# Kernel tuning notes

Measured on AMD Instinct MI355X. Metric: run time of the kernel, lower is better.

Reference implementation:

```python
import jax, jax.numpy as jnp
from jax import lax
import numpy as np

B, T = 32, 15
THR1, THR2 = 15.0, 10.0  # conv1_t, conv2_t


def _conv(x, w):
    # x: (B,T,C,H,W) cumulative potentials/spikes; conv applied per timestep
    b, t, c, h, wd = x.shape
    y = lax.conv_general_dilated(x.reshape(b * t, c, h, wd), w, (1, 1), 'VALID',
                                 dimension_numbers=('NCHW', 'OIHW', 'NCHW'))
    return y.reshape(b, t, *y.shape[1:])


def _pool(x, k, s):
    b, t, c, h, wd = x.shape
    y = lax.reduce_window(x.reshape(b * t, c, h, wd), -jnp.inf, lax.max,
                          (1, 1, k, k), (1, 1, s, s), 'VALID')
    return y.reshape(b, t, *y.shape[1:])


def _pad(x, p):
    return jnp.pad(x, ((0, 0), (0, 0), (0, 0), (p, p), (p, p)))


def _fire(pot, thr):
    # sf.fire: F.threshold_(pot, thr, 0); spk = sign
    th = jnp.where(pot > thr, pot, 0.0)
    return jnp.sign(th), th


def _winner_class(pot, spk):
    # sf.get_k_winners(pot, kwta=1, r=0, spk): earliest spike, tie-break by potential
    b, t = spk.shape[:2]
    cnt = spk.sum(axis=1)                                   # (B,F,H,W) spike counts
    first = jnp.clip((t - cnt).astype(jnp.int32), 0, t - 1)  # earliest spike time
    vals = jnp.take_along_axis(pot, first[:, None], axis=1)[:, 0]  # pot at spike time
    trunc = spk * vals[:, None]                              # (B,T,F,H,W)
    v = trunc.reshape(b, -1).max(axis=1) * t                 # dominance offset per sample
    total = (trunc + spk * v[:, None, None, None, None]).sum(axis=1)  # (B,F,H,W)
    flat = total.reshape(b, -1)
    idx = jnp.argmax(flat, axis=1)
    mx = jnp.max(flat, axis=1)
    hw = pot.shape[-1] * pot.shape[-2]
    feat = idx // hw
    # decision_map: 10 classes x 20 features each -> class = feat // 20; -1 if no spike
    return jnp.where(mx != 0, feat // 20, -1).astype(jnp.int32)


def setup_inputs() -> dict:
    key = jax.random.key(0)
    k1, k2, k3, k4 = jax.random.split(key, 4)
    # cumulative binary spike wave: neuron fires at t_fire and stays 1 afterwards
    t_fire = jax.random.randint(k1, (B, 18, 32, 32), 0, T + 1)
    inp = (jnp.arange(T)[None, :, None, None, None] >= t_fire[:, None]).astype(jnp.float32)
    w1 = 0.8 + 0.05 * jax.random.normal(k2, (90, 18, 7, 7), dtype=jnp.float32)
    w2 = 0.8 + 0.05 * jax.random.normal(k3, (250, 90, 5, 5), dtype=jnp.float32)
    w3 = 0.8 + 0.05 * jax.random.normal(k4, (200, 250, 5, 5), dtype=jnp.float32)
    return {'input': inp, 'w1': w1, 'w2': w2, 'w3': w3, 'max_layer': 3}


def reference(input, w1, w2, w3, max_layer):
    # eval-mode forward of CIFAR10Net
    x = _pad(input, 2)                       # (B,T,18,36,36)
    spk1, pot1 = _fire(_conv(x, w1), THR1)   # (B,T,90,30,30)
    if max_layer == 1:
        return spk1, pot1
    spk2, pot2 = _fire(_conv(_pad(_pool(spk1, 2, 2), 1), w2), THR2)  # (B,T,250,13,13)
    if max_layer == 2:
        return spk2, pot2
    pot3 = _conv(_pad(_pool(spk2, 3, 3), 2), w3)   # (B,T,200,4,4)
    t = pot3.shape[1]
    mask = (jnp.arange(t) == t - 1).astype(pot3.dtype)[None, :, None, None, None]
    spk3 = jnp.sign(pot3 * mask)             # fire with threshold=None: only last step
    cls = _winner_class(pot3, spk3)          # (B,) predicted class or -1
    return cls, pot3
```

## Files before the change

kernel.cpp:

```cpp
#include <hip/hip_runtime.h>

#define NB 32
#define NT 15


__device__ __forceinline__ float gather8(const int* lst, int i, const char* wb) {
    int4 p0 = *(const int4*)(lst + i);
    int4 p1 = *(const int4*)(lst + i + 4);
    int o0 = __builtin_amdgcn_readfirstlane(p0.x);
    int o1 = __builtin_amdgcn_readfirstlane(p0.y);
    int o2 = __builtin_amdgcn_readfirstlane(p0.z);
    int o3 = __builtin_amdgcn_readfirstlane(p0.w);
    int o4 = __builtin_amdgcn_readfirstlane(p1.x);
    int o5 = __builtin_amdgcn_readfirstlane(p1.y);
    int o6 = __builtin_amdgcn_readfirstlane(p1.z);
    int o7 = __builtin_amdgcn_readfirstlane(p1.w);
    float a0 = *(const float*)(wb + o0);
    float a1 = *(const float*)(wb + o1);
    float a2 = *(const float*)(wb + o2);
    float a3 = *(const float*)(wb + o3);
    float a4 = *(const float*)(wb + o4);
    float a5 = *(const float*)(wb + o5);
    float a6 = *(const float*)(wb + o6);
    float a7 = *(const float*)(wb + o7);
    return ((a0 + a1) + (a2 + a3)) + ((a4 + a5) + (a6 + a7));
}

__device__ __forceinline__ void tr_tile(const float* __restrict__ src, float* __restrict__ dst,
                                        int F, int K, int KK, int CIN, int nkt, int t, int tid) {
    __shared__ float lds[32][33];
    int kt = t % nkt, ft = t / nkt;
    int k0 = kt * 32, f0 = ft * 32;
    int tx = tid & 31, ty = tid >> 5;
#pragma unroll
    for (int i = 0; i < 4; i++) {
        int fl = ty + 8 * i;
        int f = f0 + fl, k = k0 + tx;
        lds[fl][tx] = (f < F && k < K) ? src[(size_t)f * K + k] : 0.f;
    }
    __syncthreads();
#pragma unroll
    for (int i = 0; i < 4; i++) {
        int row = ty + 8 * i;
        int k = k0 + row, f = f0 + tx;
        if (k < K && f < F) {
            int j = (k % KK) * CIN + k / KK;
            dst[(size_t)j * F + f] = lds[tx][row];
        }
    }
}

__global__ __launch_bounds__(256) void k_pre(const float* __restrict__ inp,
                                             const float* __restrict__ w1,
                                             const float* __restrict__ w2,
                                             const float* __restrict__ w3,
                                             float* __restrict__ wT1, float* __restrict__ wT2,
                                             float* __restrict__ wT3,
                                             unsigned char* __restrict__ zmap,
                                             float* __restrict__ PosS2, float* __restrict__ PosS3,
                                             float* __restrict__ Pmin1,
                                             unsigned char* __restrict__ ft1,
                                             unsigned char* __restrict__ nzc1) {
    int blk = blockIdx.x, tid = threadIdx.x;
    if (blk < 2024) {
        const float* src; float* dst;
        int F, K, KK, CIN, nkt, t;
        if (blk < 84)       { src = w1; dst = wT1; F = 90;  K = 882;  KK = 49; CIN = 18;  nkt = 28;  t = blk; }
        else if (blk < 652) { src = w2; dst = wT2; F = 250; K = 2250; KK = 25; CIN = 90;  nkt = 71;  t = blk - 84; }
        else                { src = w3; dst = wT3; F = 200; K = 6250; KK = 25; CIN = 250; nkt = 196; t = blk - 652; }
        tr_tile(src, dst, F, K, KK, CIN, nkt, t, tid);
    } else if (blk == 2024) {
        if (tid < 90)  wT1[882 * 90 + tid] = 0.f;
        if (tid < 250) wT2[(size_t)2250 * 250 + tid] = 0.f;
        if (tid < 200) wT3[(size_t)6250 * 200 + tid] = 0.f;
    } else if (blk < 2187) {
        int idx = (blk - 2025) * 256 + tid;
        int xx = idx % 36, rest = idx / 36;
        int yy = rest % 36; int b = rest / 36;
        int z = 0;
        int x = xx - 2, y = yy - 2;
        if (x >= 0 && x < 32 && y >= 0 && y < 32) {
            const float* p = inp + (size_t)b * NT * 18 * 1024 + y * 32 + x;
#pragma unroll
            for (int c = 0; c < 18; c++) z += (p[(size_t)c * 1024] != 0.f);
        }
        zmap[idx] = (unsigned char)z;
    } else if (blk < 2212) {
        int idx = (blk - 2187) * 256 + tid;
        if (idx < 6250) {
            int f = idx / 25, pos = idx - f * 25;
            float acc = 0.f;
            for (int c = 0; c < 90; c++) acc += w2[(size_t)(f * 90 + c) * 25 + pos];
            PosS2[pos * 256 + f] = acc;
        }
    } else if (blk < 2232) {
        int idx = (blk - 2212) * 256 + tid;
        if (idx < 5000) {
            int f = idx / 25, pos = idx - f * 25;
            float acc = 0.f;
            for (int c = 0; c < 250; c++) acc += w3[(size_t)(f * 250 + c) * 25 + pos];
            PosS3[pos * 200 + f] = acc;
        }
    } else if (blk < 2272) {
        int bb = blk - 2232;
        __shared__ float wm[4];
        float m = 1e30f;
#pragma unroll
        for (int k = 0; k < 8; k++) {
            int i = bb * 2048 + k * 256 + tid;
            if (i < 90 * 882) m = fminf(m, w1[i]);
        }
        for (int o = 32; o > 0; o >>= 1) m = fminf(m, __shfl_down(m, o));
        if ((tid & 63) == 0) wm[tid >> 6] = m;
        __syncthreads();
        if (tid == 0) Pmin1[bb] = fminf(fminf(wm[0], wm[1]), fminf(wm[2], wm[3]));
    } else if (blk < 2905) {
        int i = (blk - 2272) * 256 + tid;
        if (i < 162000) ((uint4*)ft1)[i] = uint4{0, 0, 0, 0};
    } else {
        int i = (blk - 2905) * 256 + tid;
        if (i < 1800) ((uint4*)nzc1)[i] = uint4{0, 0, 0, 0};
    }
}

__global__ __launch_bounds__(256) void k_conv1(const float* __restrict__ inp,
                                               const unsigned char* __restrict__ zmap,
                                               const float* __restrict__ Pmin1,
                                               const float* __restrict__ wT1,
                                               const float* __restrict__ PosS2,
                                               const float* __restrict__ PosS3,
                                               unsigned char* __restrict__ ft1,
                                               unsigned char* __restrict__ nzc1,
                                               float* __restrict__ W2e,
                                               unsigned char* __restrict__ ft2,
                                               unsigned char* __restrict__ nzc2,
                                               float* __restrict__ W3s) {
    __shared__ __align__(16) int slist[896];
    __shared__ int scnt, spcnt, cnt0s;
    __shared__ float sm1;
    int blk = blockIdx.x, tid = threadIdx.x;
    if (blk < 28800) {
        int b = blk / 900, p = blk - b * 900;
        int oy = p / 30, ox = p - oy * 30;
        int zv = 0;
        if (tid < 49) zv = zmap[(b * 36 + oy + tid / 7) * 36 + ox + tid % 7];
        float mm = (tid < 40) ? Pmin1[tid] : 1e30f;
        if (tid < 64) {
            for (int o = 32; o > 0; o >>= 1) {
                zv += __shfl_down(zv, o);
                mm = fminf(mm, __shfl_down(mm, o));
            }
            if (tid == 0) { cnt0s = zv; sm1 = mm; }
        }
        __syncthreads();
        if ((float)cnt0s * sm1 > 15.0f) return;
        unsigned char myft[4];
#pragma unroll
        for (int k = 0; k < 4; k++) {
            int j = tid + k * 256;
            unsigned char v = 255;
            if (j < 882) {
                int dy = j / 126, rem = j - dy * 126;
                int dx = rem / 18, c = rem - dx * 18;
                int y = oy + dy - 2, x = ox + dx - 2;
                v = 15;
                if ((unsigned)y < 32u && (unsigned)x < 32u)
                    v = (inp[(size_t)b * 276480 + (size_t)c * 1024 + y * 32 + x] != 0.f) ? 0 : 200;
            }
            myft[k] = v;
        }
        int f = tid < 90 ? tid : 89;
        const char* wb = (const char*)(wT1 + f);
        const int zoff = 882 * 90 * 4;
        float acc = 0.f; int ftv = 15;
        for (int s = 0; s < 15; s++) {
            if (s == 1) {
#pragma unroll
                for (int k = 0; k < 4; k++) {
                    if (myft[k] == 200) {
                        int j = tid + k * 256;
                        int dy = j / 126, rem = j - dy * 126;
                        int dx = rem / 18, c = rem - dx * 18;
                        int y = oy + dy - 2, x = ox + dx - 2;
                        const float* q = inp + (size_t)b * 276480 + (size_t)c * 1024 + y * 32 + x;
                        int cf = 0;
#pragma unroll
                        for (int t = 1; t < NT; t++) cf += (q[(size_t)t * 18432] != 0.f);
                        myft[k] = (unsigned char)(15 - cf);
                    }
                }
            }
            if (tid == 0) scnt = 0;
            __syncthreads();
#pragma unroll
            for (int k = 0; k < 4; k++) {
                if ((int)myft[k] == s) { int pp = atomicAdd(&scnt, 1); slist[pp] = (tid + k * 256) * 360; }
            }
            __syncthreads();
            if (tid == 0) {
                int c0 = scnt, cp = (c0 + 7) & ~7;
                for (int i = c0; i < cp; i++) slist[i] = zoff;
                spcnt = cp;
            }
            __syncthreads();
            int e = spcnt;
            for (int i = 0; i < e; i += 8) acc += gather8(slist, i, wb);
            if (ftv == 15 && acc > 15.0f) ftv = s;
            if (__syncthreads_and(ftv != 15)) break;
        }
        if (tid < 90) {
            ft1[(size_t)blk * 90 + tid] = (unsigned char)ftv;
            if (ftv != 0) nzc1[blk] = 1;
        }
    } else if (blk < 28969) {
        int p = blk - 28800;
        int oy = p / 13, ox = p - oy * 13;
        int f = tid < 250 ? tid : 249;
        float W = 0.f;
#pragma unroll
        for (int pos = 0; pos < 25; pos++) {
            int r = pos / 5, x = pos - r * 5;
            int gy = oy + r, gx = ox + x;
            if (!(gy == 0 || gy == 16 || gx == 0 || gx == 16)) W += PosS2[pos * 256 + f];
        }
        if (tid < 250) W2e[p * 256 + tid] = W;
        unsigned char v = (W > 10.0f) ? 0 : 15;
        if (tid < 250)
            for (int b = 0; b < NB; b++) ft2[(size_t)(b * 169 + p) * 250 + tid] = v;
        int nz = (tid < 250 && W <= 10.0f) ? 1 : 0;
        int any = __syncthreads_or(nz);
        if (tid < NB) nzc2[tid * 169 + p] = (unsigned char)any;
    } else {
        int px = blk - 28969;
        int f = tid < 200 ? tid : 199;
        int oy = px >> 2, ox = px & 3;
        int r0 = max(0, 2 - oy), r1 = min(4, 5 - oy);
        int x0 = max(0, 2 - ox), x1 = min(4, 5 - ox);
        float s = 0.f;
        for (int r = r0; r <= r1; r++)
            for (int x = x0; x <= x1; x++) s += PosS3[(r * 5 + x) * 200 + f];
        if (tid < 200) W3s[px * 200 + tid] = s;
    }
}

__global__ __launch_bounds__(256) void k_conv2(const unsigned char* __restrict__ ft1,
                                               const unsigned char* __restrict__ nzc1,
                                               const float* __restrict__ wT2,
                                               const float* __restrict__ W2e,
                                               const float* __restrict__ W3s,
                                               unsigned char* __restrict__ ft2,
                                               unsigned char* __restrict__ nzc2,
                                               float* __restrict__ out) {
    constexpr int PADCAP = 2250 + 15 * 8;
    __shared__ __align__(16) int perm[PADCAP];
    __shared__ int start[16], cur[16];
    __shared__ int cntCs, anynz;
    int blk = blockIdx.x, tid = threadIdx.x;
    if (blk >= 5408) {
        int i = (blk - 5408) * 256 + tid;
        int g = i * 4;
        int px0 = g & 15;
        int f = (g >> 4) % 200;
        float4 v;
        v.x = W3s[(px0 + 0) * 200 + f];
        v.y = W3s[(px0 + 1) * 200 + f];
        v.z = W3s[(px0 + 2) * 200 + f];
        v.w = W3s[(px0 + 3) * 200 + f];
        *(float4*)(out + 32 + (size_t)g) = v;
        return;
    }
    int idx = blk;
    int b = idx / 169, p = idx - b * 169;
    int oy = p / 13, ox = p - oy * 13;
    int gy0 = max(1, oy), gy1 = min(15, oy + 4);
    int gx0 = max(1, ox), gx1 = min(15, ox + 4);
    int y0 = 2 * (gy0 - 1), y1 = 2 * (gy1 - 1) + 1;
    int x0 = 2 * (gx0 - 1), x1 = 2 * (gx1 - 1) + 1;
    int Wd = x1 - x0 + 1, cells = (y1 - y0 + 1) * Wd;
    const unsigned char* nb = nzc1 + b * 900;
    int v = 0;
    if (tid < cells) { int yy = y0 + tid / Wd, xx = x0 + tid % Wd; v = nb[yy * 30 + xx]; }
    int dirty = __syncthreads_or(v);
    if (!dirty) return;
    const unsigned char* fb = ft1 + (size_t)b * 81000;
    if (tid == 0) { cntCs = 0; anynz = 0; }
    if (tid < 16) cur[tid] = 0;
    unsigned char myft[9];
    int nc = 0;
#pragma unroll
    for (int k = 0; k < 9; k++) {
        int j = tid + k * 256;
        myft[k] = 0;
        if (j < 2250) {
            int r = j / 450, rem = j - r * 450;
            int x = rem / 90, c = rem - x * 90;
            int gy = oy + r, gx = ox + x;
            if (gy >= 1 && gy <= 15 && gx >= 1 && gx <= 15) {
                const unsigned char* q = fb + ((size_t)((gy - 1) * 2) * 30 + (gx - 1) * 2) * 90 + c;
                int m = q[0];
                m = min(m, (int)q[90]);
                m = min(m, (int)q[2700]);
                m = min(m, (int)q[2790]);
                myft[k] = (unsigned char)m;
            }
        }
        nc += (myft[k] >= 1);
    }
    for (int o = 32; o > 0; o >>= 1) nc += __shfl_down(nc, o);
    __syncthreads();
    if ((tid & 63) == 0) atomicAdd(&cntCs, nc);
    __syncthreads();
    int f = tid < 250 ? tid : 249;
    float W = W2e[p * 256 + f];
    int ftv;
    if (cntCs == 0) {
        ftv = (W > 10.0f) ? 0 : 15;
    } else {
#pragma unroll
        for (int k = 0; k < 9; k++) { int vv = myft[k]; if (vv >= 1) atomicAdd(&cur[vv - 1], 1); }
        __syncthreads();
        if (tid == 0) {
            int s = 0;
#pragma unroll
            for (int j = 0; j < 15; j++) { int c = cur[j]; start[j] = s; s += (c + 7) & ~7; }
            start[15] = s;
        }
        __syncthreads();
        int nnzp = start[15];
        if (tid < 15) cur[tid] = start[tid];
        const int zoff = 2250 * 250 * 4;
        for (int i = tid; i < nnzp; i += 256) perm[i] = zoff;
        __syncthreads();
#pragma unroll
        for (int k = 0; k < 9; k++) {
            int vv = myft[k];
            if (vv >= 1) { int pp = atomicAdd(&cur[vv - 1], 1); perm[pp] = (tid + k * 256) * 1000; }
        }
        __syncthreads();
        const char* wb = (const char*)(wT2 + f);
        float R = 0.f; int ft = 15;
        for (int j = 14; j >= 0; j--) {
            int sjb = start[j], e = start[j + 1];
            for (int i = sjb; i < e; i += 8) R += gather8(perm, i, wb);
            float pot = W - R;
            if (pot > 10.0f) ft = j;
            if (sjb == 0) { if (pot > 10.0f) ft = 0; break; }
            if (__all(pot <= 10.0f)) break;
        }
        ftv = ft;
    }
    if (tid < 250) {
        ft2[(size_t)idx * 250 + tid] = (unsigned char)ftv;
        if (ftv != 0) anynz = 1;
    }
    __syncthreads();
    if (tid == 0) nzc2[idx] = (unsigned char)(anynz ? 1 : 0);
}

__global__ __launch_bounds__(256) void k_conv3(const unsigned char* __restrict__ ft2,
                                               const unsigned char* __restrict__ nzc2,
                                               const float* __restrict__ wT3,
                                               const float* __restrict__ W3s,
                                               float* __restrict__ out) {
    constexpr int PADCAP = 4000 + 15 * 8;
    __shared__ __align__(16) int perm[PADCAP];
    __shared__ int start[16], cur[16];
    __shared__ int fbs[16], rowb[16];
    int blk = blockIdx.x, tid = threadIdx.x;
    int idx = blk;
    int b = idx >> 4, p = idx & 15;
    int oy = p >> 2, ox = p & 3;
    int r0 = max(0, 2 - oy), r1 = min(4, 5 - oy);
    int x0 = max(0, 2 - ox), x1 = min(4, 5 - ox);
    int py0 = oy + r0 - 2, py1 = oy + r1 - 2;
    int qx0 = ox + x0 - 2, qx1 = ox + x1 - 2;
    int sy0 = 3 * py0, sy1 = 3 * py1 + 2;
    int sx0 = 3 * qx0, sx1 = 3 * qx1 + 2;
    int Wd = sx1 - sx0 + 1, cells = (sy1 - sy0 + 1) * Wd;
    const unsigned char* nb2 = nzc2 + b * 169;
    int v = 0;
    if (tid < cells) { int yy = sy0 + tid / Wd, xx = sx0 + tid % Wd; v = nb2[yy * 13 + xx]; }
    int dirty = __syncthreads_or(v);
    if (!dirty) return;
    int VR = r1 - r0 + 1, VC = x1 - x0 + 1;
    int NP = VR * VC, NV = NP * 250;
    const unsigned char* fb = ft2 + (size_t)b * 42250;
    if (tid < NP) {
        int rv = tid / VC, xv = tid - rv * VC;
        int py = oy + r0 + rv - 2, pxx = ox + x0 + xv - 2;
        fbs[tid]  = (py * 3 * 13 + pxx * 3) * 250;
        rowb[tid] = ((r0 + rv) * 5 + (x0 + xv)) * 250;
    }
    if (tid < 16) cur[tid] = 0;
    __syncthreads();
    unsigned char myft[16];
#pragma unroll
    for (int k = 0; k < 16; k++) {
        int i = tid + k * 256;
        myft[k] = 0;
        if (i < NV) {
            int posv = i / 250, c = i - posv * 250;
            const unsigned char* q = fb + fbs[posv] + c;
            int m = q[0];
#pragma unroll
            for (int dy = 0; dy < 3; dy++)
#pragma unroll
                for (int dx = 0; dx < 3; dx++)
                    if (dy | dx) m = min(m, (int)q[(dy * 13 + dx) * 250]);
            myft[k] = (unsigned char)m;
        }
    }
#pragma unroll
    for (int k = 0; k < 16; k++) { int vv = myft[k]; if (vv >= 1) atomicAdd(&cur[vv - 1], 1); }
    __syncthreads();
    if (tid == 0) {
        int s = 0;
#pragma unroll
        for (int j = 0; j < 15; j++) { int c = cur[j]; start[j] = s; s += (c + 7) & ~7; }
        start[15] = s;
    }
    __syncthreads();
    int nnzp = start[15];
    if (tid < 15) cur[tid] = start[tid];
    const int zoff = 6250 * 200 * 4;
    for (int i = tid; i < nnzp; i += 256) perm[i] = zoff;
    __syncthreads();
#pragma unroll
    for (int k = 0; k < 16; k++) {
        int vv = myft[k];
        if (vv >= 1) {
            int i = tid + k * 256;
            int posv = i / 250, c = i - posv * 250;
            int pp = atomicAdd(&cur[vv - 1], 1);
            perm[pp] = (rowb[posv] + c) * 800;
        }
    }
    __syncthreads();

    int f = tid < 200 ? tid : 199;
    const char* wb = (const char*)(wT3 + f);
    float W = W3s[p * 200 + f];
    float* o = out + 32 + ((size_t)b * NT) * 3200 + f * 16 + p;
    float R = 0.f;
    for (int j = 14; j >= 0; j--) {
        int sjb = start[j], e = start[j + 1];
        for (int i = sjb; i < e; i += 8) R += gather8(perm, i, wb);
        float pot = W - R;
        if (tid < 200) o[(size_t)j * 3200] = pot;
        if (sjb == 0) {
            for (int jj = j - 1; jj >= 0; jj--)
                if (tid < 200) o[(size_t)jj * 3200] = pot;
            break;
        }
    }
}

__global__ __launch_bounds__(256) void k_winner(const float* __restrict__ outp,
                                                float* __restrict__ outc) {
    int b = blockIdx.x, tid = threadIdx.x;
    const float* p14 = outp + 32 + ((size_t)b * NT + 14) * 3200;
    __shared__ float sv[256];
    __shared__ int   si[256];
    float m = 0.f;
    for (int j = tid; j < 3200; j += 256) {
        float v = p14[j];
        if (v > 0.f && v > m) m = v;
    }
    sv[tid] = m;
    __syncthreads();
    for (int s = 128; s > 0; s >>= 1) {
        if (tid < s) sv[tid] = fmaxf(sv[tid], sv[tid + s]);
        __syncthreads();
    }
    float vofs = 15.f * sv[0];
    __syncthreads();
    float bestv = 0.f; int besti = 0x3fffffff;
    for (int j = tid; j < 3200; j += 256) {
        float v = p14[j];
        float tot = (v > 0.f) ? v + vofs : 0.f;
        if (tot > bestv) { bestv = tot; besti = j; }
    }
    sv[tid] = bestv; si[tid] = besti;
    __syncthreads();
    for (int s = 128; s > 0; s >>= 1) {
        if (tid < s) {
            if (sv[tid + s] > sv[tid] || (sv[tid + s] == sv[tid] && si[tid + s] < si[tid])) {
                sv[tid] = sv[tid + s]; si[tid] = si[tid + s];
            }
        }
        __syncthreads();
    }
    if (tid == 0) {
        float mx = sv[0];
        int cls = (mx != 0.f) ? ((si[0] / 16) / 20) : -1;
        outc[b] = (float)cls;
    }
}

extern "C" void kernel_launch(void* const* d_in, const int* in_sizes, int n_in,
                              void* d_out, int out_size, void* d_ws, size_t ws_size,
                              hipStream_t stream) {
    const float* inp = (const float*)d_in[0];
    const float* w1  = (const float*)d_in[1];
    const float* w2  = (const float*)d_in[2];
    const float* w3  = (const float*)d_in[3];
    float* out = (float*)d_out;

    unsigned char* ws   = (unsigned char*)d_ws;
    unsigned char* ft1  = ws + 0;
    unsigned char* ft2  = ws + 2592000;
    float* wT1   = (float*)(ws + 3944000);
    float* wT2   = (float*)(ws + 4261888);
    float* wT3   = (float*)(ws + 6512896);
    float* PosS2 = (float*)(ws + 11513728);
    float* PosS3 = (float*)(ws + 11539328);
    float* W2e   = (float*)(ws + 11559328);
    float* W3s   = (float*)(ws + 11732384);
    float* Pmin1 = (float*)(ws + 11745184);
    unsigned char* zmap = ws + 11745440;
    unsigned char* nzc1 = ws + 11786912;
    unsigned char* nzc2 = ws + 11815712;

    hipLaunchKernelGGL(k_pre, dim3(2913), dim3(256), 0, stream,
                       inp, w1, w2, w3, wT1, wT2, wT3, zmap, PosS2, PosS3, Pmin1, ft1, nzc1);
    hipLaunchKernelGGL(k_conv1, dim3(28985), dim3(256), 0, stream,
                       inp, zmap, Pmin1, wT1, PosS2, PosS3, ft1, nzc1, W2e, ft2, nzc2, W3s);
    hipLaunchKernelGGL(k_conv2, dim3(6908), dim3(256), 0, stream,
                       ft1, nzc1, wT2, W2e, W3s, ft2, nzc2, out);
    hipLaunchKernelGGL(k_conv3, dim3(512), dim3(256), 0, stream, ft2, nzc2, wT3, W3s, out);
    hipLaunchKernelGGL(k_winner, dim3(NB), dim3(256), 0, stream, out, out);
}
```

Before: 156.9 us.

## Compact active conv1 pixels into a work list and fuse conv3 with winner

k_pre now does the zero-count and weight-minimum early-exit test per sample in shared memory. It appends only the conv1 output pixels that may fire to a global list, using an atomic counter. k_conv1 becomes a persistent 512-block loop over that list, so it no longer launches one block per pixel, most of which would exit immediately. Per-batch and global nonzero flags let conv2 skip whole samples and let conv3 skip its work. conv3 is merged with the winner reduction into one block per sample, which removes a launch but runs the 16 output pixels one after another, with much less parallelism when conv3 does real work.

Measured after the change: 144.4 us. 1.09x faster.

```diff
diff --git a/kernel.cpp b/kernel.cpp
--- a/kernel.cpp
+++ b/kernel.cpp
@@ -56,11 +56,10 @@
                                              const float* __restrict__ w3,
                                              float* __restrict__ wT1, float* __restrict__ wT2,
                                              float* __restrict__ wT3,
-                                             unsigned char* __restrict__ zmap,
                                              float* __restrict__ PosS2, float* __restrict__ PosS3,
-                                             float* __restrict__ Pmin1,
                                              unsigned char* __restrict__ ft1,
-                                             unsigned char* __restrict__ nzc1) {
+                                             unsigned char* __restrict__ nzc1,
+                                             int* __restrict__ cnt, int* __restrict__ list1) {
     int blk = blockIdx.x, tid = threadIdx.x;
     if (blk < 2024) {
         const float* src; float* dst;
@@ -73,147 +72,165 @@
         if (tid < 90)  wT1[882 * 90 + tid] = 0.f;
         if (tid < 250) wT2[(size_t)2250 * 250 + tid] = 0.f;
         if (tid < 200) wT3[(size_t)6250 * 200 + tid] = 0.f;
-    } else if (blk < 2187) {
+    } else if (blk < 2050) {
         int idx = (blk - 2025) * 256 + tid;
-        int xx = idx % 36, rest = idx / 36;
-        int yy = rest % 36; int b = rest / 36;
-        int z = 0;
-        int x = xx - 2, y = yy - 2;
-        if (x >= 0 && x < 32 && y >= 0 && y < 32) {
-            const float* p = inp + (size_t)b * NT * 18 * 1024 + y * 32 + x;
-#pragma unroll
-            for (int c = 0; c < 18; c++) z += (p[(size_t)c * 1024] != 0.f);
-        }
-        zmap[idx] = (unsigned char)z;
-    } else if (blk < 2212) {
-        int idx = (blk - 2187) * 256 + tid;
         if (idx < 6250) {
             int f = idx / 25, pos = idx - f * 25;
             float acc = 0.f;
             for (int c = 0; c < 90; c++) acc += w2[(size_t)(f * 90 + c) * 25 + pos];
             PosS2[pos * 256 + f] = acc;
         }
-    } else if (blk < 2232) {
-        int idx = (blk - 2212) * 256 + tid;
+    } else if (blk < 2070) {
+        int idx = (blk - 2050) * 256 + tid;
         if (idx < 5000) {
             int f = idx / 25, pos = idx - f * 25;
             float acc = 0.f;
             for (int c = 0; c < 250; c++) acc += w3[(size_t)(f * 250 + c) * 25 + pos];
             PosS3[pos * 200 + f] = acc;
         }
-    } else if (blk < 2272) {
-        int bb = blk - 2232;
-        __shared__ float wm[4];
+    } else if (blk < 2703) {
+        int i = (blk - 2070) * 256 + tid;
+        if (i < 162000) ((uint4*)ft1)[i] = uint4{0, 0, 0, 0};
+    } else if (blk < 2712) {
+        int i = (blk - 2703) * 256 + tid;
+        if (i < 2143) ((uint4*)nzc1)[i] = uint4{0, 0, 0, 0};
+    } else {
+        int b = blk - 2712;
+        __shared__ unsigned char zl[36][36];
+        __shared__ unsigned short rs[36][30];
+        __shared__ float wm4[4];
+        __shared__ float m1s;
+        for (int i = tid; i < 1296; i += 256) ((unsigned char*)zl)[i] = 0;
+        __syncthreads();
+#pragma unroll
+        for (int k = 0; k < 4; k++) {
+            int pix = tid + k * 256;
+            int y = pix >> 5, x = pix & 31;
+            const float* p = inp + (size_t)b * 276480 + y * 32 + x;
+            int z = 0;
+#pragma unroll
+            for (int c = 0; c < 18; c++) z += (p[(size_t)c * 1024] != 0.f);
+            zl[y + 2][x + 2] = (unsigned char)z;
+        }
         float m = 1e30f;
-#pragma unroll
-        for (int k = 0; k < 8; k++) {
-            int i = bb * 2048 + k * 256 + tid;
-            if (i < 90 * 882) m = fminf(m, w1[i]);
+        const float4* w4 = (const float4*)w1;
+        for (int i = tid; i < 19845; i += 256) {
+            float4 v = w4[i];
+            m = fminf(m, fminf(fminf(v.x, v.y), fminf(v.z, v.w)));
         }
         for (int o = 32; o > 0; o >>= 1) m = fminf(m, __shfl_down(m, o));
-        if ((tid & 63) == 0) wm[tid >> 6] = m;
-        __syncthreads();
-        if (tid == 0) Pmin1[bb] = fminf(fminf(wm[0], wm[1]), fminf(wm[2], wm[3]));
-    } else if (blk < 2905) {
-        int i = (blk - 2272) * 256 + tid;
-        if (i < 162000) ((uint4*)ft1)[i] = uint4{0, 0, 0, 0};
-    } else {
-        int i = (blk - 2905) * 256 + tid;
-        if (i < 1800) ((uint4*)nzc1)[i] = uint4{0, 0, 0, 0};
+        if ((tid & 63) == 0) wm4[tid >> 6] = m;
+        __syncthreads();
+        if (tid == 0) m1s = fminf(fminf(wm4[0], wm4[1]), fminf(wm4[2], wm4[3]));
+        __syncthreads();
+        for (int i = tid; i < 1080; i += 256) {
+            int y = i / 30, x = i - (i / 30) * 30;
+            int s = 0;
+#pragma unroll
+            for (int d = 0; d < 7; d++) s += zl[y][x + d];
+            rs[y][x] = (unsigned short)s;
+        }
+        __syncthreads();
+        float m1 = m1s;
+        for (int i = tid; i < 900; i += 256) {
+            int oy = i / 30, ox = i - (i / 30) * 30;
+            int s = 0;
+#pragma unroll
+            for (int d = 0; d < 7; d++) s += rs[oy + d][ox];
+            if (!((float)s * m1 > 15.0f)) {
+                int pos = atomicAdd(cnt, 1);
+                list1[pos] = b * 900 + i;
+            }
+        }
     }
 }
 
 __global__ __launch_bounds__(256) void k_conv1(const float* __restrict__ inp,
-                                               const unsigned char* __restrict__ zmap,
-                                               const float* __restrict__ Pmin1,
                                                const float* __restrict__ wT1,
                                                const float* __restrict__ PosS2,
                                                const float* __restrict__ PosS3,
+                                               const int* __restrict__ cnt,
+                                               const int* __restrict__ list1,
                                                unsigned char* __restrict__ ft1,
                                                unsigned char* __restrict__ nzc1,
+                                               unsigned char* __restrict__ nzb1,
                                                float* __restrict__ W2e,
                                                unsigned char* __restrict__ ft2,
                                                unsigned char* __restrict__ nzc2,
+                                               int* __restrict__ nzg2,
                                                float* __restrict__ W3s) {
     __shared__ __align__(16) int slist[896];
-    __shared__ int scnt, spcnt, cnt0s;
-    __shared__ float sm1;
+    __shared__ int scnt, spcnt;
     int blk = blockIdx.x, tid = threadIdx.x;
-    if (blk < 28800) {
-        int b = blk / 900, p = blk - b * 900;
-        int oy = p / 30, ox = p - oy * 30;
-        int zv = 0;
-        if (tid < 49) zv = zmap[(b * 36 + oy + tid / 7) * 36 + ox + tid % 7];
-        float mm = (tid < 40) ? Pmin1[tid] : 1e30f;
-        if (tid < 64) {
-            for (int o = 32; o > 0; o >>= 1) {
-                zv += __shfl_down(zv, o);
-                mm = fminf(mm, __shfl_down(mm, o));
-            }
-            if (tid == 0) { cnt0s = zv; sm1 = mm; }
-        }
-        __syncthreads();
-        if ((float)cnt0s * sm1 > 15.0f) return;
-        unsigned char myft[4];
-#pragma unroll
-        for (int k = 0; k < 4; k++) {
-            int j = tid + k * 256;
-            unsigned char v = 255;
-            if (j < 882) {
-                int dy = j / 126, rem = j - dy * 126;
-                int dx = rem / 18, c = rem - dx * 18;
-                int y = oy + dy - 2, x = ox + dx - 2;
-                v = 15;
-                if ((unsigned)y < 32u && (unsigned)x < 32u)
-                    v = (inp[(size_t)b * 276480 + (size_t)c * 1024 + y * 32 + x] != 0.f) ? 0 : 200;
-            }
-            myft[k] = v;
-        }
-        int f = tid < 90 ? tid : 89;
-        const char* wb = (const char*)(wT1 + f);
-        const int zoff = 882 * 90 * 4;
-        float acc = 0.f; int ftv = 15;
-        for (int s = 0; s < 15; s++) {
-            if (s == 1) {
+    if (blk < 512) {
+        int n1 = cnt[0];
+        for (int it = blk; it < n1; it += 512) {
+            __syncthreads();
+            int idx = list1[it];
+            int b = idx / 900, p = idx - b * 900;
+            int oy = p / 30, ox = p - oy * 30;
+            unsigned char myft[4];
+#pragma unroll
+            for (int k = 0; k < 4; k++) {
+                int j = tid + k * 256;
+                unsigned char v = 255;
+                if (j < 882) {
+                    int dy = j / 126, rem = j - dy * 126;
+                    int dx = rem / 18, c = rem - dx * 18;
+                    int y = oy + dy - 2, x = ox + dx - 2;
+                    v = 15;
+                    if ((unsigned)y < 32u && (unsigned)x < 32u)
+                        v = (inp[(size_t)b * 276480 + (size_t)c * 1024 + y * 32 + x] != 0.f) ? 0 : 200;
+                }
+                myft[k] = v;
+            }
+            int f = tid < 90 ? tid : 89;
+            const char* wb = (const char*)(wT1 + f);
+            const int zoff = 882 * 90 * 4;
+            float acc = 0.f; int ftv = 15;
+            for (int s = 0; s < 15; s++) {
+                if (s == 1) {
+#pragma unroll
+                    for (int k = 0; k < 4; k++) {
+                        if (myft[k] == 200) {
+                            int j = tid + k * 256;
+                            int dy = j / 126, rem = j - dy * 126;
+                            int dx = rem / 18, c = rem - dx * 18;
+                            int y = oy + dy - 2, x = ox + dx - 2;
+                            const float* q = inp + (size_t)b * 276480 + (size_t)c * 1024 + y * 32 + x;
+                            int cf = 0;
+#pragma unroll
+                            for (int t = 1; t < NT; t++) cf += (q[(size_t)t * 18432] != 0.f);
+                            myft[k] = (unsigned char)(15 - cf);
+                        }
+                    }
+                }
+                if (tid == 0) scnt = 0;
+                __syncthreads();
 #pragma unroll
                 for (int k = 0; k < 4; k++) {
-                    if (myft[k] == 200) {
-                        int j = tid + k * 256;
-                        int dy = j / 126, rem = j - dy * 126;
-                        int dx = rem / 18, c = rem - dx * 18;
-                        int y = oy + dy - 2, x = ox + dx - 2;
-                        const float* q = inp + (size_t)b * 276480 + (size_t)c * 1024 + y * 32 + x;
-                        int cf = 0;
-#pragma unroll
-                        for (int t = 1; t < NT; t++) cf += (q[(size_t)t * 18432] != 0.f);
-                        myft[k] = (unsigned char)(15 - cf);
-                    }
-                }
-            }
-            if (tid == 0) scnt = 0;
-            __syncthreads();
-#pragma unroll
-            for (int k = 0; k < 4; k++) {
-                if ((int)myft[k] == s) { int pp = atomicAdd(&scnt, 1); slist[pp] = (tid + k * 256) * 360; }
-            }
-            __syncthreads();
-            if (tid == 0) {
-                int c0 = scnt, cp = (c0 + 7) & ~7;
-                for (int i = c0; i < cp; i++) slist[i] = zoff;
-                spcnt = cp;
-            }
-            __syncthreads();
-            int e = spcnt;
-            for (int i = 0; i < e; i += 8) acc += gather8(slist, i, wb);
-            if (ftv == 15 && acc > 15.0f) ftv = s;
-            if (__syncthreads_and(ftv != 15)) break;
-        }
-        if (tid < 90) {
-            ft1[(size_t)blk * 90 + tid] = (unsigned char)ftv;
-            if (ftv != 0) nzc1[blk] = 1;
-        }
-    } else if (blk < 28969) {
-        int p = blk - 28800;
+                    if ((int)myft[k] == s) { int pp = atomicAdd(&scnt, 1); slist[pp] = (tid + k * 256) * 360; }
+                }
+                __syncthreads();
+                if (tid == 0) {
+                    int c0 = scnt, cp = (c0 + 7) & ~7;
+                    for (int i = c0; i < cp; i++) slist[i] = zoff;
+                    spcnt = cp;
+                }
+                __syncthreads();
+                int e = spcnt;
+                for (int i = 0; i < e; i += 8) acc += gather8(slist, i, wb);
+                if (ftv == 15 && acc > 15.0f) ftv = s;
+                if (__syncthreads_and(ftv != 15)) break;
+            }
+            if (tid < 90) {
+                ft1[(size_t)idx * 90 + tid] = (unsigned char)ftv;
+                if (ftv != 0) { nzc1[idx] = 1; nzb1[b] = 1; }
+            }
+            __syncthreads();
+        }
+    } else if (blk < 681) {
+        int p = blk - 512;
         int oy = p / 13, ox = p - oy * 13;
         int f = tid < 250 ? tid : 249;
         float W = 0.f;
@@ -230,8 +247,9 @@
         int nz = (tid < 250 && W <= 10.0f) ? 1 : 0;
         int any = __syncthreads_or(nz);
         if (tid < NB) nzc2[tid * 169 + p] = (unsigned char)any;
+        if (tid == 0 && any) *nzg2 = 1;
     } else {
-        int px = blk - 28969;
+        int px = blk - 681;
         int f = tid < 200 ? tid : 199;
         int oy = px >> 2, ox = px & 3;
         int r0 = max(0, 2 - oy), r1 = min(4, 5 - oy);
@@ -245,11 +263,13 @@
 
 __global__ __launch_bounds__(256) void k_conv2(const unsigned char* __restrict__ ft1,
                                                const unsigned char* __restrict__ nzc1,
+                                               const unsigned char* __restrict__ nzb1,
                                                const float* __restrict__ wT2,
                                                const float* __restrict__ W2e,
                                                const float* __restrict__ W3s,
                                                unsigned char* __restrict__ ft2,
                                                unsigned char* __restrict__ nzc2,
+                                               unsigned char* __restrict__ nzb2,
                                                float* __restrict__ out) {
     constexpr int PADCAP = 2250 + 15 * 8;
     __shared__ __align__(16) int perm[PADCAP];
@@ -271,6 +291,7 @@
     }
     int idx = blk;
     int b = idx / 169, p = idx - b * 169;
+    if (nzb1[b] == 0) return;
     int oy = p / 13, ox = p - oy * 13;
     int gy0 = max(1, oy), gy1 = min(15, oy + 4);
     int gx0 = max(1, ox), gx1 = min(15, ox + 4);
@@ -354,113 +375,118 @@
         if (ftv != 0) anynz = 1;
     }
     __syncthreads();
-    if (tid == 0) nzc2[idx] = (unsigned char)(anynz ? 1 : 0);
-}
-
-__global__ __launch_bounds__(256) void k_conv3(const unsigned char* __restrict__ ft2,
-                                               const unsigned char* __restrict__ nzc2,
-                                               const float* __restrict__ wT3,
-                                               const float* __restrict__ W3s,
-                                               float* __restrict__ out) {
+    if (tid == 0) {
+        nzc2[idx] = (unsigned char)(anynz ? 1 : 0);
+        if (anynz) nzb2[b] = 1;
+    }
+}
+
+__global__ __launch_bounds__(256) void k_conv3w(const unsigned char* __restrict__ ft2,
+                                                const unsigned char* __restrict__ nzc2,
+                                                const unsigned char* __restrict__ nzb2,
+                                                const int* __restrict__ nzg2,
+                                                const float* __restrict__ wT3,
+                                                const float* __restrict__ W3s,
+                                                float* __restrict__ out) {
     constexpr int PADCAP = 4000 + 15 * 8;
     __shared__ __align__(16) int perm[PADCAP];
     __shared__ int start[16], cur[16];
     __shared__ int fbs[16], rowb[16];
-    int blk = blockIdx.x, tid = threadIdx.x;
-    int idx = blk;
-    int b = idx >> 4, p = idx & 15;
-    int oy = p >> 2, ox = p & 3;
-    int r0 = max(0, 2 - oy), r1 = min(4, 5 - oy);
-    int x0 = max(0, 2 - ox), x1 = min(4, 5 - ox);
-    int py0 = oy + r0 - 2, py1 = oy + r1 - 2;
-    int qx0 = ox + x0 - 2, qx1 = ox + x1 - 2;
-    int sy0 = 3 * py0, sy1 = 3 * py1 + 2;
-    int sx0 = 3 * qx0, sx1 = 3 * qx1 + 2;
-    int Wd = sx1 - sx0 + 1, cells = (sy1 - sy0 + 1) * Wd;
-    const unsigned char* nb2 = nzc2 + b * 169;
-    int v = 0;
-    if (tid < cells) { int yy = sy0 + tid / Wd, xx = sx0 + tid % Wd; v = nb2[yy * 13 + xx]; }
-    int dirty = __syncthreads_or(v);
-    if (!dirty) return;
-    int VR = r1 - r0 + 1, VC = x1 - x0 + 1;
-    int NP = VR * VC, NV = NP * 250;
-    const unsigned char* fb = ft2 + (size_t)b * 42250;
-    if (tid < NP) {
-        int rv = tid / VC, xv = tid - rv * VC;
-        int py = oy + r0 + rv - 2, pxx = ox + x0 + xv - 2;
-        fbs[tid]  = (py * 3 * 13 + pxx * 3) * 250;
-        rowb[tid] = ((r0 + rv) * 5 + (x0 + xv)) * 250;
-    }
-    if (tid < 16) cur[tid] = 0;
-    __syncthreads();
-    unsigned char myft[16];
-#pragma unroll
-    for (int k = 0; k < 16; k++) {
-        int i = tid + k * 256;
-        myft[k] = 0;
-        if (i < NV) {
-            int posv = i / 250, c = i - posv * 250;
-            const unsigned char* q = fb + fbs[posv] + c;
-            int m = q[0];
-#pragma unroll
-            for (int dy = 0; dy < 3; dy++)
-#pragma unroll
-                for (int dx = 0; dx < 3; dx++)
-                    if (dy | dx) m = min(m, (int)q[(dy * 13 + dx) * 250]);
-            myft[k] = (unsigned char)m;
-        }
-    }
-#pragma unroll
-    for (int k = 0; k < 16; k++) { int vv = myft[k]; if (vv >= 1) atomicAdd(&cur[vv - 1], 1); }
-    __syncthreads();
-    if (tid == 0) {
-        int s = 0;
-#pragma unroll
-        for (int j = 0; j < 15; j++) { int c = cur[j]; start[j] = s; s += (c + 7) & ~7; }
-        start[15] = s;
-    }
-    __syncthreads();
-    int nnzp = start[15];
-    if (tid < 15) cur[tid] = start[tid];
-    const int zoff = 6250 * 200 * 4;
-    for (int i = tid; i < nnzp; i += 256) perm[i] = zoff;
-    __syncthreads();
-#pragma unroll
-    for (int k = 0; k < 16; k++) {
-        int vv = myft[k];
-        if (vv >= 1) {
-            int i = tid + k * 256;
-            int posv = i / 250, c = i - posv * 250;
-            int pp = atomicAdd(&cur[vv - 1], 1);
-            perm[pp] = (rowb[posv] + c) * 800;
-        }
-    }
-    __syncthreads();
-
-    int f = tid < 200 ? tid : 199;
-    const char* wb = (const char*)(wT3 + f);
-    float W = W3s[p * 200 + f];
-    float* o = out + 32 + ((size_t)b * NT) * 3200 + f * 16 + p;
-    float R = 0.f;
-    for (int j = 14; j >= 0; j--) {
-        int sjb = start[j], e = start[j + 1];
-        for (int i = sjb; i < e; i += 8) R += gather8(perm, i, wb);
-        float pot = W - R;
-        if (tid < 200) o[(size_t)j * 3200] = pot;
-        if (sjb == 0) {
-            for (int jj = j - 1; jj >= 0; jj--)
-                if (tid < 200) o[(size_t)jj * 3200] = pot;
-            break;
-        }
-    }
-}
-
-__global__ __launch_bounds__(256) void k_winner(const float* __restrict__ outp,
-                                                float* __restrict__ outc) {
-    int b = blockIdx.x, tid = threadIdx.x;
-    const float* p14 = outp + 32 + ((size_t)b * NT + 14) * 3200;
     __shared__ float sv[256];
     __shared__ int   si[256];
+    int b = blockIdx.x, tid = threadIdx.x;
+    int maybe = nzg2[0] | (int)nzb2[b];
+    if (maybe) {
+        for (int p = 0; p < 16; p++) {
+            int oy = p >> 2, ox = p & 3;
+            int r0 = max(0, 2 - oy), r1 = min(4, 5 - oy);
+            int x0 = max(0, 2 - ox), x1 = min(4, 5 - ox);
+            int py0 = oy + r0 - 2, py1 = oy + r1 - 2;
+            int qx0 = ox + x0 - 2, qx1 = ox + x1 - 2;
+            int sy0 = 3 * py0, sy1 = 3 * py1 + 2;
+            int sx0 = 3 * qx0, sx1 = 3 * qx1 + 2;
+            int Wd = sx1 - sx0 + 1, cells = (sy1 - sy0 + 1) * Wd;
+            const unsigned char* nb2 = nzc2 + b * 169;
+            int v = 0;
+            if (tid < cells) { int yy = sy0 + tid / Wd, xx = sx0 + tid % Wd; v = nb2[yy * 13 + xx]; }
+            int dirty = __syncthreads_or(v);
+            if (!dirty) continue;
+            int VR = r1 - r0 + 1, VC = x1 - x0 + 1;
+            int NP = VR * VC, NV = NP * 250;
+            const unsigned char* fb = ft2 + (size_t)b * 42250;
+            if (tid < NP) {
+                int rv = tid / VC, xv = tid - rv * VC;
+                int py = oy + r0 + rv - 2, pxx = ox + x0 + xv - 2;
+                fbs[tid]  = (py * 3 * 13 + pxx * 3) * 250;
+                rowb[tid] = ((r0 + rv) * 5 + (x0 + xv)) * 250;
+            }
+            if (tid < 16) cur[tid] = 0;
+            __syncthreads();
+            unsigned char myft[16];
+#pragma unroll
+            for (int k = 0; k < 16; k++) {
+                int i = tid + k * 256;
+                myft[k] = 0;
+                if (i < NV) {
+                    int posv = i / 250, c = i - posv * 250;
+                    const unsigned char* q = fb + fbs[posv] + c;
+                    int m = q[0];
+#pragma unroll
+                    for (int dy = 0; dy < 3; dy++)
+#pragma unroll
+                        for (int dx = 0; dx < 3; dx++)
+                            if (dy | dx) m = min(m, (int)q[(dy * 13 + dx) * 250]);
+                    myft[k] = (unsigned char)m;
+                }
+            }
+#pragma unroll
+            for (int k = 0; k < 16; k++) { int vv = myft[k]; if (vv >= 1) atomicAdd(&cur[vv - 1], 1); }
+            __syncthreads();
+            if (tid == 0) {
+                int s = 0;
+#pragma unroll
+                for (int j = 0; j < 15; j++) { int c = cur[j]; start[j] = s; s += (c + 7) & ~7; }
+                start[15] = s;
+            }
+            __syncthreads();
+            int nnzp = start[15];
+            if (tid < 15) cur[tid] = start[tid];
+            const int zoff = 6250 * 200 * 4;
+            for (int i = tid; i < nnzp; i += 256) perm[i] = zoff;
+            __syncthreads();
+#pragma unroll
+            for (int k = 0; k < 16; k++) {
+                int vv = myft[k];
+                if (vv >= 1) {
+                    int i = tid + k * 256;
+                    int posv = i / 250, c = i - posv * 250;
+                    int pp = atomicAdd(&cur[vv - 1], 1);
+                    perm[pp] = (rowb[posv] + c) * 800;
+                }
+            }
+            __syncthreads();
+
+            int f = tid < 200 ? tid : 199;
+            const char* wb = (const char*)(wT3 + f);
+            float W = W3s[p * 200 + f];
+            float* o = out + 32 + ((size_t)b * NT) * 3200 + f * 16 + p;
+            float R = 0.f;
+            for (int j = 14; j >= 0; j--) {
+                int sjb = start[j], e = start[j + 1];
+                for (int i = sjb; i < e; i += 8) R += gather8(perm, i, wb);
+                float pot = W - R;
+                if (tid < 200) o[(size_t)j * 3200] = pot;
+                if (sjb == 0) {
+                    for (int jj = j - 1; jj >= 0; jj--)
+                        if (tid < 200) o[(size_t)jj * 3200] = pot;
+                    break;
+                }
+            }
+            __syncthreads();
+        }
+    }
+    __syncthreads();
+    const float* p14 = out + 32 + ((size_t)b * NT + 14) * 3200;
     float m = 0.f;
     for (int j = tid; j < 3200; j += 256) {
         float v = p14[j];
@@ -493,7 +519,7 @@
     if (tid == 0) {
         float mx = sv[0];
         int cls = (mx != 0.f) ? ((si[0] / 16) / 20) : -1;
-        outc[b] = (float)cls;
+        out[b] = (float)cls;
     }
 }
 
@@ -516,17 +542,21 @@
     float* PosS3 = (float*)(ws + 11539328);
     float* W2e   = (float*)(ws + 11559328);
     float* W3s   = (float*)(ws + 11732384);
-    float* Pmin1 = (float*)(ws + 11745184);
-    unsigned char* zmap = ws + 11745440;
     unsigned char* nzc1 = ws + 11786912;
     unsigned char* nzc2 = ws + 11815712;
-
-    hipLaunchKernelGGL(k_pre, dim3(2913), dim3(256), 0, stream,
-                       inp, w1, w2, w3, wT1, wT2, wT3, zmap, PosS2, PosS3, Pmin1, ft1, nzc1);
-    hipLaunchKernelGGL(k_conv1, dim3(28985), dim3(256), 0, stream,
-                       inp, zmap, Pmin1, wT1, PosS2, PosS3, ft1, nzc1, W2e, ft2, nzc2, W3s);
+    unsigned char* nzb1 = ws + 11821120;
+    unsigned char* nzb2 = ws + 11821152;
+    int* nzg2  = (int*)(ws + 11821184);
+    int* cnt   = (int*)(ws + 11821200);
+    int* list1 = (int*)(ws + 11821312);
+
+    hipMemsetAsync(cnt, 0, 16, stream);
+    hipLaunchKernelGGL(k_pre, dim3(2744), dim3(256), 0, stream,
+                       inp, w1, w2, w3, wT1, wT2, wT3, PosS2, PosS3, ft1, nzc1, cnt, list1);
+    hipLaunchKernelGGL(k_conv1, dim3(697), dim3(256), 0, stream,
+                       inp, wT1, PosS2, PosS3, cnt, list1, ft1, nzc1, nzb1, W2e, ft2, nzc2, nzg2, W3s);
     hipLaunchKernelGGL(k_conv2, dim3(6908), dim3(256), 0, stream,
-                       ft1, nzc1, wT2, W2e, W3s, ft2, nzc2, out);
-    hipLaunchKernelGGL(k_conv3, dim3(512), dim3(256), 0, stream, ft2, nzc2, wT3, W3s, out);
-    hipLaunchKernelGGL(k_winner, dim3(NB), dim3(256), 0, stream, out, out);
-}
+                       ft1, nzc1, nzb1, wT2, W2e, W3s, ft2, nzc2, nzb2, out);
+    hipLaunchKernelGGL(k_conv3w, dim3(NB), dim3(256), 0, stream,
+                       ft2, nzc2, nzb2, nzg2, wT3, W3s, out);
+}
```
